# Optimization experiments

Measured on AMD Instinct MI355X. Metric: run time of the kernel, lower is better.

## Reference

```python
import jax, jax.numpy as jnp
import numpy as np

B = 4096
D = 256
N = 9000000
ALPHA = 0.5      # alpha_weight
GAMMA_S = 0.8
GAMMA_U = 0.9
RHO = 6.0
EPS = 1e-14
ETA = 0.01
TAU_MIN = 0.001
TAU_MAX = 1.0
GRAD_CLIP = 5.0
TAU_INIT = 0.07


def setup_inputs() -> dict:
    key = jax.random.key(0)
    k1, k2 = jax.random.split(key)
    return {
        "zis": jax.random.normal(k1, (B, D), dtype=jnp.float32),
        "zjs": jax.random.normal(k2, (B, D), dtype=jnp.float32),
        "ids": jnp.arange(B, dtype=jnp.int32),
        "s_I": jnp.zeros(N, jnp.float32),
        "s_T": jnp.zeros(N, jnp.float32),
        "b_I": jnp.zeros(N, jnp.float32),
        "b_T": jnp.zeros(N, jnp.float32),
        "u_I": jnp.zeros(N, jnp.float32),
        "u_T": jnp.zeros(N, jnp.float32),
        "tau_I": jnp.full(N, TAU_INIT, jnp.float32),
        "tau_T": jnp.full(N, TAU_INIT, jnp.float32),
    }


def reference(zis, zjs, ids, s_I, s_T, b_I, b_T, u_I, u_T, tau_I, tau_T):
    sg = jax.lax.stop_gradient
    Bc = zis.shape[0]
    # normalize
    zis = zis / jnp.linalg.norm(zis, axis=1, keepdims=True)
    zjs = zjs / jnp.linalg.norm(zjs, axis=1, keepdims=True)
    sim = jnp.einsum('id,jd->ij', zis, zjs)                 # [B,B]
    diag = jnp.diagonal(sim)
    image_diffs = sim - diag[:, None]
    text_diffs = sim - diag[None, :]
    tau_i = tau_I[ids]
    tau_t = tau_T[ids]
    # detached temperature-scaled diffs (torch .detach())
    idt = sg(image_diffs) / tau_i[:, None]
    tdt = sg(text_diffs) / tau_t[None, :]
    # running max update (online log-sum-exp shift)
    old_b_i = b_I[ids]
    old_b_t = b_T[ids]
    new_b_i = jnp.maximum(old_b_i, idt.max(axis=1))
    new_b_t = jnp.maximum(old_b_t, tdt.max(axis=0))
    mask = 1.0 - jnp.eye(Bc, dtype=zis.dtype)
    exp_i = jnp.exp(idt - new_b_i[:, None]) * mask
    exp_t = jnp.exp(tdt - new_b_t[None, :]) * mask
    g_i = exp_i.sum(axis=1)                                  # [B]
    g_t = exp_t.sum(axis=0)                                  # [B]
    # EMA of normalizers, rescaled by max shift
    s_i = (1.0 - GAMMA_S) * s_I[ids] * jnp.exp(old_b_i - new_b_i) + GAMMA_S * g_i
    s_t = (1.0 - GAMMA_S) * s_T[ids] * jnp.exp(old_b_t - new_b_t) + GAMMA_S * g_t
    s_i_c = jnp.clip(s_i, EPS, None)[:, None]                # [B,1]
    s_t_c = jnp.clip(s_t, EPS, None)[None, :]                # [1,B]
    w_i = exp_i / s_i_c
    w_t = exp_t / s_t_c
    image_loss = (sg(w_i) * image_diffs).sum(axis=1)         # [B]
    text_loss = (sg(w_t) * text_diffs).sum(axis=0)           # [B]
    total_loss = ALPHA * image_loss.mean() + (1.0 - ALPHA) * text_loss.mean()
    grad_tau_image = jnp.log(s_i_c) + new_b_i[:, None] + RHO - (w_i * idt).sum(axis=1, keepdims=True) / (Bc - 1)
    grad_tau_text = jnp.log(s_t_c) + new_b_t[None, :] + RHO - (w_t * tdt).sum(axis=0, keepdims=True) / (Bc - 1)
    # EMA of tau gradients with clipping, then temperature update
    u_i = (1.0 - GAMMA_U) * u_I[ids] + GAMMA_U * jnp.clip(grad_tau_image[:, 0], -GRAD_CLIP, GRAD_CLIP)
    u_t = (1.0 - GAMMA_U) * u_T[ids] + GAMMA_U * jnp.clip(grad_tau_text[0, :], -GRAD_CLIP, GRAD_CLIP)
    tau_i_new = jnp.clip(tau_i - ETA * u_i, TAU_MIN, TAU_MAX)
    tau_t_new = jnp.clip(tau_t - ETA * u_t, TAU_MIN, TAU_MAX)
    # scatter updated state back into persistent buffers
    s_I = s_I.at[ids].set(s_i)
    s_T = s_T.at[ids].set(s_t)
    b_I = b_I.at[ids].set(new_b_i)
    b_T = b_T.at[ids].set(new_b_t)
    u_I = u_I.at[ids].set(u_i)
    u_T = u_T.at[ids].set(u_t)
    tau_I = tau_I.at[ids].set(tau_i_new)
    tau_T = tau_T.at[ids].set(tau_t_new)
    return (g_i[:, None], g_t[None, :], grad_tau_image, grad_tau_text, total_loss,
            tau_i.mean(), tau_t.mean(), s_I, s_T, b_I, b_T, u_I, u_T, tau_I, tau_T)
```

## Files before the change

kernel.cpp:

```cpp
#include <hip/hip_runtime.h>
#include <math.h>

#define BDIM 4096
#define DDIM 256
#define NSTATE 9000000
#define PREFIX 3674116
#define BANK0_N4 1331471
#define PREFIX_N4 918529
#define COPY_THREADS 1048576

#define C_ALPHA 0.5f
#define C_GAMMA_S 0.8f
#define C_GAMMA_U 0.9f
#define C_RHO 6.0f
#define C_EPS 1e-14f
#define C_ETA 0.01f
#define C_TAU_MIN 0.001f
#define C_TAU_MAX 1.0f
#define C_GRAD_CLIP 5.0f

typedef unsigned short u16;
typedef __attribute__((ext_vector_type(8))) short short8;
typedef __attribute__((ext_vector_type(16))) float f32x16;
typedef __attribute__((ext_vector_type(4))) float nf4;

#define MFMA32 __builtin_amdgcn_mfma_f32_32x32x16_bf16

__device__ inline u16 f2bf(float f) {
    unsigned u = __float_as_uint(f);
    unsigned r = (u + 0x7FFFu + ((u >> 16) & 1u)) >> 16;
    return (u16)r;
}
__device__ inline float bf2f(u16 h) { return __uint_as_float(((unsigned)h) << 16); }

__device__ inline void nt_copy4(const nf4* __restrict__ s, long k, float* __restrict__ dbase) {
    nf4 v = __builtin_nontemporal_load(&s[k]);
    float* dp = dbase + 4 * k;
    __builtin_nontemporal_store(v.x, dp + 0);
    __builtin_nontemporal_store(v.y, dp + 1);
    __builtin_nontemporal_store(v.z, dp + 2);
    __builtin_nontemporal_store(v.w, dp + 3);
}

__global__ __launch_bounds__(256) void kprep(const float* __restrict__ zis,
                                             const float* __restrict__ zjs,
                                             u16* __restrict__ Ah, u16* __restrict__ Al,
                                             u16* __restrict__ Bh, u16* __restrict__ Bl,
                                             const int* __restrict__ ids,
                                             const float* __restrict__ tau_I,
                                             const float* __restrict__ tau_T,
                                             float* __restrict__ rowIT,
                                             float* __restrict__ colIT) {
    int blk = blockIdx.x;
    int t = threadIdx.x;
    if (blk == 256) {
        for (int i = t; i < BDIM; i += 256) {
            int id = ids[i];
            rowIT[i] = 1.0f / tau_I[id];
            colIT[i] = 1.0f / tau_T[id];
        }
        return;
    }
    bool isB = blk >= 128;
    const float* Z = isB ? zjs : zis;
    u16* H = isB ? Bh : Ah;
    u16* L = isB ? Bl : Al;
    int rblk = blk & 127;
    int r = t & 31, kc0 = t >> 5;
    int row = rblk * 32 + r;

    __shared__ float ssq[32];
    if (t < 32) ssq[t] = 0.f;
    __syncthreads();

    float4 v[8];
    float partial = 0.f;
#pragma unroll
    for (int c = 0; c < 4; ++c) {
        int kc = kc0 + 8 * c;
        float4 a = *(const float4*)&Z[(size_t)row * DDIM + kc * 8];
        float4 b = *(const float4*)&Z[(size_t)row * DDIM + kc * 8 + 4];
        v[2 * c] = a; v[2 * c + 1] = b;
        partial += a.x * a.x + a.y * a.y + a.z * a.z + a.w * a.w;
        partial += b.x * b.x + b.y * b.y + b.z * b.z + b.w * b.w;
    }
    atomicAdd(&ssq[r], partial);
    __syncthreads();
    float inv = rsqrtf(ssq[r]);

#pragma unroll
    for (int c = 0; c < 4; ++c) {
        int kc = kc0 + 8 * c;
        float f[8];
        f[0] = v[2*c].x * inv;   f[1] = v[2*c].y * inv;
        f[2] = v[2*c].z * inv;   f[3] = v[2*c].w * inv;
        f[4] = v[2*c+1].x * inv; f[5] = v[2*c+1].y * inv;
        f[6] = v[2*c+1].z * inv; f[7] = v[2*c+1].w * inv;
        u16 hh[8], ll[8];
#pragma unroll
        for (int j = 0; j < 8; ++j) {
            hh[j] = f2bf(f[j]);
            ll[j] = f2bf(f[j] - bf2f(hh[j]));
        }
        size_t base = (size_t)rblk * 8192 + (size_t)kc * 256 + (size_t)r * 8;
        uint4 ph, pl;
        ph.x = (unsigned)hh[0] | ((unsigned)hh[1] << 16);
        ph.y = (unsigned)hh[2] | ((unsigned)hh[3] << 16);
        ph.z = (unsigned)hh[4] | ((unsigned)hh[5] << 16);
        ph.w = (unsigned)hh[6] | ((unsigned)hh[7] << 16);
        pl.x = (unsigned)ll[0] | ((unsigned)ll[1] << 16);
        pl.y = (unsigned)ll[2] | ((unsigned)ll[3] << 16);
        pl.z = (unsigned)ll[4] | ((unsigned)ll[5] << 16);
        pl.w = (unsigned)ll[6] | ((unsigned)ll[7] << 16);
        *(uint4*)(H + base) = ph;
        *(uint4*)(L + base) = pl;
    }
}

__global__ __launch_bounds__(256, 3) void kmain(
    const u16* __restrict__ Ah, const u16* __restrict__ Al,
    const u16* __restrict__ Bh, const u16* __restrict__ Bl,
    const float* __restrict__ rowIT, const float* __restrict__ colIT,
    float* __restrict__ rPM, float* __restrict__ rPS1, float* __restrict__ rPS2,
    float* __restrict__ cPM, float* __restrict__ cPS1, float* __restrict__ cPS2,
    float* __restrict__ diag,
    const float* __restrict__ s_I, const float* __restrict__ s_T,
    const float* __restrict__ b_I, const float* __restrict__ b_T,
    const float* __restrict__ u_I, const float* __restrict__ u_T,
    const float* __restrict__ tau_I, const float* __restrict__ tau_T,
    float* o)
{
    __shared__ float T[2][64 * 68];
    int bid = blockIdx.x;
    int t = threadIdx.x;

    if (bid % 5 != 0) {
        long cid = (long)(bid / 5) * 4 + (bid % 5) - 1;
        long tid = cid * 256 + t;
        {
            const nf4* s = (const nf4*)(s_I + PREFIX);
            float* d = o + PREFIX;
            for (long k = tid; k < BANK0_N4; k += COPY_THREADS) nt_copy4(s, k, d);
        }
        const float* srcs[7] = {s_T, b_I, b_T, u_I, u_T, tau_I, tau_T};
#pragma unroll
        for (int b = 0; b < 7; b++) {
            const nf4* s = (const nf4*)srcs[b];
            float* d = o + (long)(b + 1) * NSTATE;
            for (long k = tid; k < NSTATE / 4; k += COPY_THREADS) nt_copy4(s, k, d);
        }
        return;
    }

    int gid = bid / 5;
    int by = gid >> 5, bx = gid & 31;
    int w = t >> 6, l = t & 63;
    int rw = w & 1, cw = w >> 1;
    int h = l >> 5, lc = l & 31;
    int rowbase = by * 128 + rw * 64;
    int colbase = bx * 128 + cw * 64;

    const u16* pAh = Ah + (size_t)(by * 4 + rw * 2) * 8192;
    const u16* pAl = Al + (size_t)(by * 4 + rw * 2) * 8192;
    const u16* pBh = Bh + (size_t)(bx * 4 + cw * 2) * 8192;
    const u16* pBl = Bl + (size_t)(bx * 4 + cw * 2) * 8192;

    f32x16 acc00, acc01, acc10, acc11;
#pragma unroll
    for (int e = 0; e < 16; ++e) { acc00[e] = 0.f; acc01[e] = 0.f; acc10[e] = 0.f; acc11[e] = 0.f; }

    for (int s = 0; s < 16; ++s) {
        int off = s * 512 + l * 8;
        short8 a0h = *(const short8*)(pAh + off);
        short8 a1h = *(const short8*)(pAh + 8192 + off);
        short8 a0l = *(const short8*)(pAl + off);
        short8 a1l = *(const short8*)(pAl + 8192 + off);
        short8 b0h = *(const short8*)(pBh + off);
        short8 b1h = *(const short8*)(pBh + 8192 + off);
        short8 b0l = *(const short8*)(pBl + off);
        short8 b1l = *(const short8*)(pBl + 8192 + off);

        acc00 = MFMA32(a0h, b0h, acc00, 0, 0, 0);
        acc01 = MFMA32(a0h, b1h, acc01, 0, 0, 0);
        acc10 = MFMA32(a1h, b0h, acc10, 0, 0, 0);
        acc11 = MFMA32(a1h, b1h, acc11, 0, 0, 0);
        acc00 = MFMA32(a0h, b0l, acc00, 0, 0, 0);
        acc01 = MFMA32(a0h, b1l, acc01, 0, 0, 0);
        acc10 = MFMA32(a1h, b0l, acc10, 0, 0, 0);
        acc11 = MFMA32(a1h, b1l, acc11, 0, 0, 0);
        acc00 = MFMA32(a0l, b0h, acc00, 0, 0, 0);
        acc01 = MFMA32(a0l, b1h, acc01, 0, 0, 0);
        acc10 = MFMA32(a1l, b0h, acc10, 0, 0, 0);
        acc11 = MFMA32(a1l, b1h, acc11, 0, 0, 0);
    }

#define COLPART(A0, A1, CT) do {                                                   \
        int gc = colbase + (CT) * 32 + lc;                                         \
        float itc = colIT[gc];                                                     \
        float m = -INFINITY;                                                       \
        _Pragma("unroll") for (int e = 0; e < 16; ++e) {                           \
            m = fmaxf(m, (A0)[e]); m = fmaxf(m, (A1)[e]); }                        \
        m = fmaxf(m, __shfl_xor(m, 32));                                           \
        float S1 = 0.f, S2 = 0.f;                                                  \
        _Pragma("unroll") for (int e = 0; e < 16; ++e) {                           \
            float v0 = (A0)[e]; float e0 = __expf((v0 - m) * itc); S1 += e0; S2 += e0 * v0; \
            float v1 = (A1)[e]; float e1 = __expf((v1 - m) * itc); S1 += e1; S2 += e1 * v1; } \
        S1 += __shfl_xor(S1, 32); S2 += __shfl_xor(S2, 32);                        \
        if (h == 0) { int slot = by * 2 + rw;                                      \
            cPM [slot * 4096 + gc] = m;                                            \
            cPS1[slot * 4096 + gc] = S1;                                           \
            cPS2[slot * 4096 + gc] = S2; }                                         \
    } while (0)

    COLPART(acc00, acc10, 0);
    COLPART(acc01, acc11, 1);

#define ROWPART(TB) do {                                                           \
        float* Tb = (TB);                                                          \
        _Pragma("unroll") for (int q = 0; q < 4; ++q) {                            \
            _Pragma("unroll") for (int j = 0; j < 4; ++j) {                        \
                int rr = 8 * q + 4 * h + j;                                        \
                Tb[(rr     ) * 68 + lc     ] = acc00[4 * q + j];                   \
                Tb[(rr     ) * 68 + lc + 32] = acc01[4 * q + j];                   \
                Tb[(rr + 32) * 68 + lc     ] = acc10[4 * q + j];                   \
                Tb[(rr + 32) * 68 + lc + 32] = acc11[4 * q + j]; } }               \
        float itr = rowIT[rowbase + l];                                            \
        float4 vv[16];                                                             \
        _Pragma("unroll") for (int c = 0; c < 16; ++c)                             \
            vv[c] = *(const float4*)&Tb[l * 68 + 4 * c];                           \
        float m = -INFINITY;                                                       \
        _Pragma("unroll") for (int c = 0; c < 16; ++c)                             \
            m = fmaxf(m, fmaxf(fmaxf(vv[c].x, vv[c].y), fmaxf(vv[c].z, vv[c].w))); \
        float S1 = 0.f, S2 = 0.f;                                                  \
        _Pragma("unroll") for (int c = 0; c < 16; ++c) {                           \
            float e0 = __expf((vv[c].x - m) * itr); S1 += e0; S2 += e0 * vv[c].x;  \
            float e1 = __expf((vv[c].y - m) * itr); S1 += e1; S2 += e1 * vv[c].y;  \
            float e2 = __expf((vv[c].z - m) * itr); S1 += e2; S2 += e2 * vv[c].z;  \
            float e3 = __expf((vv[c].w - m) * itr); S1 += e3; S2 += e3 * vv[c].w; }\
        int slot = bx * 2 + cw;                                                    \
        rPM [slot * 4096 + rowbase + l] = m;                                       \
        rPS1[slot * 4096 + rowbase + l] = S1;                                      \
        rPS2[slot * 4096 + rowbase + l] = S2;                                      \
        if (bx == by && rw == cw) diag[rowbase + l] = Tb[l * 68 + l];              \
    } while (0)

    if (w < 2) ROWPART(T[w]);
    __syncthreads();
    if (w >= 2) ROWPART(T[w - 2]);
}

__global__ __launch_bounds__(256) void kmerge(
    const int* __restrict__ ids,
    const float* __restrict__ s_I, const float* __restrict__ b_I,
    const float* __restrict__ u_I, const float* __restrict__ tau_I,
    const float* __restrict__ s_T, const float* __restrict__ b_T,
    const float* __restrict__ u_T, const float* __restrict__ tau_T,
    const float* __restrict__ rowIT, const float* __restrict__ colIT,
    const float* __restrict__ diag,
    const float* __restrict__ rPM, const float* __restrict__ rPS1, const float* __restrict__ rPS2,
    const float* __restrict__ cPM, const float* __restrict__ cPS1, const float* __restrict__ cPS2,
    float* __restrict__ O,
    float* __restrict__ sc_arrs,
    float* __restrict__ img_loss_arr,
    float* __restrict__ txt_loss_arr)
{
    int j = blockIdx.x * 256 + threadIdx.x;
    if (j >= 2 * BDIM) return;
    bool rowside = (j < BDIM);
    int i = rowside ? j : j - BDIM;
    const float* PM  = rowside ? rPM  : cPM;
    const float* PS1 = rowside ? rPS1 : cPS1;
    const float* PS2 = rowside ? rPS2 : cPS2;
    float it = rowside ? rowIT[i] : colIT[i];

    float M = -INFINITY, S1 = 0.f, S2 = 0.f;
    for (int k = 0; k < 64; k++) {
        float m  = PM [k * BDIM + i];
        float s1 = PS1[k * BDIM + i];
        float s2 = PS2[k * BDIM + i];
        float Mn = fmaxf(M, m);
        float ea = __expf((M - Mn) * it);
        float eb = __expf((m - Mn) * it);
        S1 = S1 * ea + s1 * eb;
        S2 = S2 * ea + s2 * eb;
        M = Mn;
    }

    int id = ids[i];
    float tau  = rowside ? tau_I[id] : tau_T[id];
    float oldb = rowside ? b_I[id]   : b_T[id];
    float olds = rowside ? s_I[id]   : s_T[id];
    float oldu = rowside ? u_I[id]   : u_T[id];
    float dg = diag[i];

    float nb = fmaxf(oldb, (M - dg) * it);
    float F  = __expf((M - dg) * it - nb);
    float ed = __expf(-nb);
    float g  = F * S1 - ed;
    float Cs = F * (S2 - dg * S1);

    float s_new = (1.f - C_GAMMA_S) * olds * __expf(oldb - nb) + C_GAMMA_S * g;
    float sc = fmaxf(s_new, C_EPS);
    float loss = Cs / sc;
    float grad = logf(sc) + nb + C_RHO - (Cs / (sc * tau)) * (1.0f / (float)(BDIM - 1));
    float gc = fminf(fmaxf(grad, -C_GRAD_CLIP), C_GRAD_CLIP);
    float u_new = (1.f - C_GAMMA_U) * oldu + C_GAMMA_U * gc;
    float tau_new = fminf(fmaxf(tau - C_ETA * u_new, C_TAU_MIN), C_TAU_MAX);

    if (rowside) {
        O[i] = g;
        O[8192 + i] = grad;
        sc_arrs[0 * BDIM + i] = s_new;
        sc_arrs[1 * BDIM + i] = nb;
        sc_arrs[2 * BDIM + i] = u_new;
        sc_arrs[3 * BDIM + i] = tau_new;
        img_loss_arr[i] = loss;
    } else {
        O[4096 + i] = g;
        O[12288 + i] = grad;
        sc_arrs[4 * BDIM + i] = s_new;
        sc_arrs[5 * BDIM + i] = nb;
        sc_arrs[6 * BDIM + i] = u_new;
        sc_arrs[7 * BDIM + i] = tau_new;
        txt_loss_arr[i] = loss;
    }
}

__global__ __launch_bounds__(256) void kfix(const float* s_I, float* o,
                                            const float* img_loss_arr,
                                            const float* txt_loss_arr,
                                            const int* ids,
                                            const float* tau_I, const float* tau_T,
                                            float* O) {
    int bid = blockIdx.x;
    int t = threadIdx.x;
    if (bid < 3584) {
        long tid = (long)bid * 256 + t;
        const nf4* s = (const nf4*)s_I;
        for (long k = tid; k < PREFIX_N4; k += 3584L * 256) nt_copy4(s, k, o);
        return;
    }
    float s0 = 0.f, s1 = 0.f, s2 = 0.f, s3 = 0.f;
    for (int k = t; k < BDIM; k += 256) {
        s0 += img_loss_arr[k];
        s1 += txt_loss_arr[k];
        int id = ids[k];
        s2 += tau_I[id];
        s3 += tau_T[id];
    }
    __shared__ float r0[256], r1[256], r2[256], r3[256];
    r0[t] = s0; r1[t] = s1; r2[t] = s2; r3[t] = s3;
    __syncthreads();
    for (int s = 128; s > 0; s >>= 1) {
        if (t < s) {
            r0[t] += r0[t + s]; r1[t] += r1[t + s];
            r2[t] += r2[t + s]; r3[t] += r3[t + s];
        }
        __syncthreads();
    }
    if (t == 0) {
        float invB = 1.0f / (float)BDIM;
        O[16384] = C_ALPHA * (r0[0] * invB) + (1.f - C_ALPHA) * (r1[0] * invB);
        O[16385] = r2[0] * invB;
        O[16386] = r3[0] * invB;
    }
}

__global__ __launch_bounds__(256) void kscat(const int* __restrict__ ids,
                                             const float* __restrict__ sc_arrs,
                                             float* __restrict__ o) {
    int t = blockIdx.x * 256 + threadIdx.x;
    if (t >= BDIM) return;
    long id = ids[t];
    o[0L * NSTATE + id] = sc_arrs[0 * BDIM + t];
    o[1L * NSTATE + id] = sc_arrs[4 * BDIM + t];
    o[2L * NSTATE + id] = sc_arrs[1 * BDIM + t];
    o[3L * NSTATE + id] = sc_arrs[5 * BDIM + t];
    o[4L * NSTATE + id] = sc_arrs[2 * BDIM + t];
    o[5L * NSTATE + id] = sc_arrs[6 * BDIM + t];
    o[6L * NSTATE + id] = sc_arrs[3 * BDIM + t];
    o[7L * NSTATE + id] = sc_arrs[7 * BDIM + t];
}

extern "C" void kernel_launch(void* const* d_in, const int* in_sizes, int n_in,
                              void* d_out, int out_size, void* d_ws, size_t ws_size,
                              hipStream_t stream) {
    const float* zis   = (const float*)d_in[0];
    const float* zjs   = (const float*)d_in[1];
    const int*   ids   = (const int*)d_in[2];
    const float* s_I   = (const float*)d_in[3];
    const float* s_T   = (const float*)d_in[4];
    const float* b_I   = (const float*)d_in[5];
    const float* b_T   = (const float*)d_in[6];
    const float* u_I   = (const float*)d_in[7];
    const float* u_T   = (const float*)d_in[8];
    const float* tau_I = (const float*)d_in[9];
    const float* tau_T = (const float*)d_in[10];
    float* O  = (float*)d_out;
    float* ws = (float*)d_ws;

    float* P = O + 16388;
    float* rPM  = P;
    float* rPS1 = P + 262144;
    float* rPS2 = P + 524288;
    float* cPM  = P + 786432;
    float* cPS1 = P + 1048576;
    float* cPS2 = P + 1310720;
    float* diag = P + 1572864;
    u16* AB = (u16*)(P + 1576960);
    u16* Ah = AB;
    u16* Al = AB + 1048576;
    u16* Bh = AB + 2097152;
    u16* Bl = AB + 3145728;

    float* rowIT  = ws;
    float* colIT  = ws + 4096;
    float* sc_arrs = ws + 8192;
    float* img_loss_arr = ws + 40960;
    float* txt_loss_arr = ws + 45056;

    kprep<<<257, 256, 0, stream>>>(zis, zjs, Ah, Al, Bh, Bl,
                                   ids, tau_I, tau_T, rowIT, colIT);

    kmain<<<5120, 256, 0, stream>>>(Ah, Al, Bh, Bl, rowIT, colIT,
                                    rPM, rPS1, rPS2, cPM, cPS1, cPS2, diag,
                                    s_I, s_T, b_I, b_T, u_I, u_T, tau_I, tau_T,
                                    O + 16387);

    kmerge<<<32, 256, 0, stream>>>(ids, s_I, b_I, u_I, tau_I, s_T, b_T, u_T, tau_T,
                                   rowIT, colIT, diag,
                                   rPM, rPS1, rPS2, cPM, cPS1, cPS2,
                                   O, sc_arrs, img_loss_arr, txt_loss_arr);

    kfix<<<3585, 256, 0, stream>>>(s_I, O + 16387, img_loss_arr, txt_loss_arr,
                                   ids, tau_I, tau_T, O);

    kscat<<<16, 256, 0, stream>>>(ids, sc_arrs, O + 16387);
}
```

Baseline: 552.4 us.

## Move scratch partials to workspace so state copy and scatter happen in-place

When the workspace is large enough, the GEMM partials and split-precision operands are placed in workspace instead of the output tail. That lets kmain copy the whole s_I bank at once, and kmerge scatters the updated state directly into the output. The separate prefix-copy kernel and the scatter kernel are dropped in favour of a single-block scalar reduction. This removes a serialized copy pass and two launches, but it depends on ws_size and relies on kmerge's scatter being ordered after kmain's bulk copy by the stream.

```diff
diff --git a/kernel.cpp b/kernel.cpp
--- a/kernel.cpp
+++ b/kernel.cpp
@@ -5,7 +5,6 @@
 #define DDIM 256
 #define NSTATE 9000000
 #define PREFIX 3674116
-#define BANK0_N4 1331471
 #define PREFIX_N4 918529
 #define COPY_THREADS 1048576
 
@@ -128,7 +127,7 @@
     const float* __restrict__ b_I, const float* __restrict__ b_T,
     const float* __restrict__ u_I, const float* __restrict__ u_T,
     const float* __restrict__ tau_I, const float* __restrict__ tau_T,
-    float* o)
+    long b0s, float* o)
 {
     __shared__ float T[2][64 * 68];
     int bid = blockIdx.x;
@@ -138,9 +137,10 @@
         long cid = (long)(bid / 5) * 4 + (bid % 5) - 1;
         long tid = cid * 256 + t;
         {
-            const nf4* s = (const nf4*)(s_I + PREFIX);
-            float* d = o + PREFIX;
-            for (long k = tid; k < BANK0_N4; k += COPY_THREADS) nt_copy4(s, k, d);
+            const nf4* s = (const nf4*)(s_I + b0s);
+            float* d = o + b0s;
+            long n4 = (NSTATE - b0s) / 4;
+            for (long k = tid; k < n4; k += COPY_THREADS) nt_copy4(s, k, d);
         }
         const float* srcs[7] = {s_T, b_I, b_T, u_I, u_T, tau_I, tau_T};
 #pragma unroll
@@ -261,6 +261,7 @@
     const float* __restrict__ cPM, const float* __restrict__ cPS1, const float* __restrict__ cPS2,
     float* __restrict__ O,
     float* __restrict__ sc_arrs,
+    float* o_scat,
     float* __restrict__ img_loss_arr,
     float* __restrict__ txt_loss_arr)
 {
@@ -307,22 +308,61 @@
     float u_new = (1.f - C_GAMMA_U) * oldu + C_GAMMA_U * gc;
     float tau_new = fminf(fmaxf(tau - C_ETA * u_new, C_TAU_MIN), C_TAU_MAX);
 
+    int bank0 = rowside ? 0 : 1;
     if (rowside) {
         O[i] = g;
         O[8192 + i] = grad;
-        sc_arrs[0 * BDIM + i] = s_new;
-        sc_arrs[1 * BDIM + i] = nb;
-        sc_arrs[2 * BDIM + i] = u_new;
-        sc_arrs[3 * BDIM + i] = tau_new;
         img_loss_arr[i] = loss;
     } else {
         O[4096 + i] = g;
         O[12288 + i] = grad;
-        sc_arrs[4 * BDIM + i] = s_new;
-        sc_arrs[5 * BDIM + i] = nb;
-        sc_arrs[6 * BDIM + i] = u_new;
-        sc_arrs[7 * BDIM + i] = tau_new;
         txt_loss_arr[i] = loss;
+    }
+    if (o_scat) {
+        long lid = id;
+        o_scat[(long)(bank0 + 0) * NSTATE + lid] = s_new;
+        o_scat[(long)(bank0 + 2) * NSTATE + lid] = nb;
+        o_scat[(long)(bank0 + 4) * NSTATE + lid] = u_new;
+        o_scat[(long)(bank0 + 6) * NSTATE + lid] = tau_new;
+    } else {
+        int base = rowside ? 0 : 4;
+        sc_arrs[(base + 0) * BDIM + i] = s_new;
+        sc_arrs[(base + 1) * BDIM + i] = nb;
+        sc_arrs[(base + 2) * BDIM + i] = u_new;
+        sc_arrs[(base + 3) * BDIM + i] = tau_new;
+    }
+}
+
+__global__ __launch_bounds__(256) void kscal(const float* __restrict__ img_loss_arr,
+                                             const float* __restrict__ txt_loss_arr,
+                                             const int* __restrict__ ids,
+                                             const float* __restrict__ tau_I,
+                                             const float* __restrict__ tau_T,
+                                             float* __restrict__ O) {
+    int t = threadIdx.x;
+    float s0 = 0.f, s1 = 0.f, s2 = 0.f, s3 = 0.f;
+    for (int k = t; k < BDIM; k += 256) {
+        s0 += img_loss_arr[k];
+        s1 += txt_loss_arr[k];
+        int id = ids[k];
+        s2 += tau_I[id];
+        s3 += tau_T[id];
+    }
+    __shared__ float r0[256], r1[256], r2[256], r3[256];
+    r0[t] = s0; r1[t] = s1; r2[t] = s2; r3[t] = s3;
+    __syncthreads();
+    for (int s = 128; s > 0; s >>= 1) {
+        if (t < s) {
+            r0[t] += r0[t + s]; r1[t] += r1[t + s];
+            r2[t] += r2[t + s]; r3[t] += r3[t + s];
+        }
+        __syncthreads();
+    }
+    if (t == 0) {
+        float invB = 1.0f / (float)BDIM;
+        O[16384] = C_ALPHA * (r0[0] * invB) + (1.f - C_ALPHA) * (r1[0] * invB);
+        O[16385] = r2[0] * invB;
+        O[16386] = r3[0] * invB;
     }
 }
 
@@ -399,25 +439,34 @@
     float* O  = (float*)d_out;
     float* ws = (float*)d_ws;
 
-    float* P = O + 16388;
-    float* rPM  = P;
-    float* rPS1 = P + 262144;
-    float* rPS2 = P + 524288;
-    float* cPM  = P + 786432;
-    float* cPS1 = P + 1048576;
-    float* cPS2 = P + 1310720;
-    float* diag = P + 1572864;
-    u16* AB = (u16*)(P + 1576960);
-    u16* Ah = AB;
-    u16* Al = AB + 1048576;
-    u16* Bh = AB + 2097152;
-    u16* Bl = AB + 3145728;
-
     float* rowIT  = ws;
     float* colIT  = ws + 4096;
-    float* sc_arrs = ws + 8192;
-    float* img_loss_arr = ws + 40960;
-    float* txt_loss_arr = ws + 45056;
+    float* img_loss_arr = ws + 8192;
+    float* txt_loss_arr = ws + 12288;
+    float* sc_arrs = ws + 16384;
+
+    const bool bigws = ws_size >= (size_t)16 * 1024 * 1024;
+
+    float *rPM, *rPS1, *rPS2, *cPM, *cPS1, *cPS2, *diag;
+    u16 *Ah, *Al, *Bh, *Bl;
+    long b0s;
+    if (bigws) {
+        float* P = ws + 53248;
+        rPM  = P;            rPS1 = P + 262144;  rPS2 = P + 524288;
+        cPM  = P + 786432;   cPS1 = P + 1048576; cPS2 = P + 1310720;
+        diag = P + 1572864;
+        Ah = (u16*)(P + 1576960);
+        Al = Ah + 1048576; Bh = Al + 1048576; Bl = Bh + 1048576;
+        b0s = 0;
+    } else {
+        float* P = O + 16388;
+        rPM  = P;            rPS1 = P + 262144;  rPS2 = P + 524288;
+        cPM  = P + 786432;   cPS1 = P + 1048576; cPS2 = P + 1310720;
+        diag = P + 1572864;
+        Ah = (u16*)(P + 1576960);
+        Al = Ah + 1048576; Bh = Al + 1048576; Bl = Bh + 1048576;
+        b0s = PREFIX;
+    }
 
     kprep<<<257, 256, 0, stream>>>(zis, zjs, Ah, Al, Bh, Bl,
                                    ids, tau_I, tau_T, rowIT, colIT);
@@ -425,15 +474,19 @@
     kmain<<<5120, 256, 0, stream>>>(Ah, Al, Bh, Bl, rowIT, colIT,
                                     rPM, rPS1, rPS2, cPM, cPS1, cPS2, diag,
                                     s_I, s_T, b_I, b_T, u_I, u_T, tau_I, tau_T,
-                                    O + 16387);
+                                    b0s, O + 16387);
 
     kmerge<<<32, 256, 0, stream>>>(ids, s_I, b_I, u_I, tau_I, s_T, b_T, u_T, tau_T,
                                    rowIT, colIT, diag,
                                    rPM, rPS1, rPS2, cPM, cPS1, cPS2,
-                                   O, sc_arrs, img_loss_arr, txt_loss_arr);
-
-    kfix<<<3585, 256, 0, stream>>>(s_I, O + 16387, img_loss_arr, txt_loss_arr,
-                                   ids, tau_I, tau_T, O);
-
-    kscat<<<16, 256, 0, stream>>>(ids, sc_arrs, O + 16387);
-}
+                                   O, sc_arrs, bigws ? (O + 16387) : nullptr,
+                                   img_loss_arr, txt_loss_arr);
+
+    if (bigws) {
+        kscal<<<1, 256, 0, stream>>>(img_loss_arr, txt_loss_arr, ids, tau_I, tau_T, O);
+    } else {
+        kfix<<<3585, 256, 0, stream>>>(s_I, O + 16387, img_loss_arr, txt_loss_arr,
+                                       ids, tau_I, tau_T, O);
+        kscat<<<16, 256, 0, stream>>>(ids, sc_arrs, O + 16387);
+    }
+}
```

New measurement: 547.2 us. Within noise of the previous version (-0.9%).
